# Kernel optimization log

Hardware: AMD Instinct MI355X
Metric: run time of the kernel (lower is better)

## Reference

```python
import jax, jax.numpy as jnp
import numpy as np

BZ, DC, NR = 65536, 512, 1024
MARGIN = 1.0
MASK_VAL = 1000.0

def _l2_normalize(x, eps=1e-12):
    # F.normalize: x / max(||x||_2, eps) along last dim
    n = jnp.sqrt(jnp.sum(x * x, axis=-1, keepdims=True))
    return x / jnp.maximum(n, eps)

def setup_inputs() -> dict:
    key = jax.random.key(0)
    k1, k2, k3 = jax.random.split(key, 3)
    wo = jax.random.normal(k1, (BZ, DC), dtype=jnp.float32)
    rel_weight = jax.random.normal(k2, (NR, DC), dtype=jnp.float32)
    in_y = jax.random.randint(k3, (BZ,), 0, NR, dtype=jnp.int64)
    return {"wo": wo, "rel_weight": rel_weight, "in_y": in_y}

def reference(wo, rel_weight, in_y):
    wo_n = _l2_normalize(wo)                       # [bz, dc]
    rw_n = _l2_normalize(rel_weight)               # [nr, dc]
    # ||a-b|| for unit vectors: sqrt(2 - 2 a.b); avoids [bz,nr,dc] intermediate
    sim = jnp.einsum('bd,nd->bn', wo_n, rw_n)      # [bz, nr]
    all_distance = jnp.sqrt(jnp.maximum(2.0 - 2.0 * sim, 0.0))
    b = jnp.arange(wo.shape[0])
    masked = all_distance.at[b, in_y].add(MASK_VAL)  # mask out the true class
    neg_idx = jnp.argmin(masked, axis=1)           # nearest wrong relation
    # gather instead of one-hot matmul; dist to gathered row equals row of all_distance
    pos_distance = all_distance[b, in_y]
    neg_distance = all_distance[b, neg_idx]
    loss = jnp.mean(pos_distance + jnp.clip(MARGIN - neg_distance, 0.0, 9999.0))
    return loss
```

## Files before the change

kernel.cpp:

```cpp
#include <hip/hip_runtime.h>
#include <hip/hip_bf16.h>
#include <stdint.h>

#define BZc 65536
#define DCc 512
#define NRc 1024

#define BM 128
#define BNC 128
#define BKC 64
#define A_BYTES (BM * DCc * 2)
#define B_BYTES (BNC * BKC * 2)
#define SMEM_BYTES (A_BYTES + B_BYTES + 512 + 512 + 512 + 16)

typedef __bf16 bf16x8 __attribute__((ext_vector_type(8)));
typedef float f32x4 __attribute__((ext_vector_type(4)));

__device__ __forceinline__ unsigned short f2bf(float f) {
    unsigned int u = __float_as_uint(f);
    return (unsigned short)((u + 0x7FFFu + ((u >> 16) & 1u)) >> 16);
}

__global__ void __launch_bounds__(64) ndl_prep_kernel(const float* __restrict__ rw,
                                                      unsigned short* __restrict__ rwn,
                                                      float* __restrict__ out) {
    if (blockIdx.x == 0 && threadIdx.x == 0) out[0] = 0.0f;
    const int t = threadIdx.x;
    const int row = blockIdx.x * 8 + (t >> 3);
    const int l8 = t & 7;
    const float4* src = (const float4*)(rw + (size_t)row * DCc);
    float4 v[16];
    float ss = 0.0f;
#pragma unroll
    for (int i = 0; i < 16; ++i) {
        v[i] = src[l8 + 8 * i];
        ss += v[i].x * v[i].x + v[i].y * v[i].y + v[i].z * v[i].z + v[i].w * v[i].w;
    }
    ss += __shfl_xor(ss, 1);
    ss += __shfl_xor(ss, 2);
    ss += __shfl_xor(ss, 4);
    const float inv = rsqrtf(fmaxf(ss, 1e-24f));
    ushort4* dst = (ushort4*)(rwn + (size_t)row * DCc);
#pragma unroll
    for (int i = 0; i < 16; ++i) {
        ushort4 u;
        u.x = f2bf(v[i].x * inv); u.y = f2bf(v[i].y * inv);
        u.z = f2bf(v[i].z * inv); u.w = f2bf(v[i].w * inv);
        dst[l8 + 8 * i] = u;
    }
}

__global__ void __launch_bounds__(256) ndl_main_kernel(const float* __restrict__ wo,
                                                       const unsigned short* __restrict__ rwn,
                                                       const long long* __restrict__ iy,
                                                       float* __restrict__ out) {
    extern __shared__ char smem[];
    char* Ab = smem;
    char* Bb = smem + A_BYTES;
    unsigned int* rowmax = (unsigned int*)(smem + A_BYTES + B_BYTES);
    float* simY = (float*)(smem + A_BYTES + B_BYTES + 512);
    int* yv = (int*)(smem + A_BYTES + B_BYTES + 1024);
    float* redsum = (float*)(smem + A_BYTES + B_BYTES + 1536);

    const int t = threadIdx.x;
    const int rbase = blockIdx.x * BM;

    if (t < BM) {
        rowmax[t] = 0u;
        simY[t] = 0.0f;
        yv[t] = (int)iy[rbase + t];
    }

    {
        const int l8 = t & 7;
#pragma unroll 1
        for (int p = 0; p < 4; ++p) {
            const int rloc = p * 32 + (t >> 3);
            const float4* src = (const float4*)(wo + (size_t)(rbase + rloc) * DCc);
            float4 v[16];
            float ss = 0.0f;
#pragma unroll
            for (int i = 0; i < 16; ++i) {
                v[i] = src[l8 + 8 * i];
                ss += v[i].x * v[i].x + v[i].y * v[i].y + v[i].z * v[i].z + v[i].w * v[i].w;
            }
            ss += __shfl_xor(ss, 1);
            ss += __shfl_xor(ss, 2);
            ss += __shfl_xor(ss, 4);
            const float inv = rsqrtf(fmaxf(ss, 1e-24f));
            const int swz = (rloc & 7) << 4;
            char* rowp = Ab + rloc * (DCc * 2);
#pragma unroll
            for (int i = 0; i < 16; ++i) {
                ushort4 u;
                u.x = f2bf(v[i].x * inv); u.y = f2bf(v[i].y * inv);
                u.z = f2bf(v[i].z * inv); u.w = f2bf(v[i].w * inv);
                const int boff = ((l8 + 8 * i) * 8) ^ swz;
                *(ushort4*)(rowp + boff) = u;
            }
        }
    }

    const int wid = t >> 6;
    const int lane = t & 63;
    const int wm = wid >> 1;
    const int wn = wid & 1;
    const int lm = lane & 15;
    const int lk = lane >> 4;

    int a_rowbase[4], a_swz[4];
#pragma unroll
    for (int mt = 0; mt < 4; ++mt) {
        const int r = wm * 64 + mt * 16 + lm;
        a_rowbase[mt] = r * (DCc * 2);
        a_swz[mt] = (r & 7) << 4;
    }
    int b_rowbase[4], b_swz[4];
#pragma unroll
    for (int nt = 0; nt < 4; ++nt) {
        const int n = wn * 64 + nt * 16 + lm;
        b_rowbase[nt] = n * (BKC * 2);
        b_swz[nt] = (n & 7) << 4;
    }

    for (int nb = 0; nb < 8; ++nb) {
        f32x4 acc[4][4];
#pragma unroll
        for (int mt = 0; mt < 4; ++mt)
#pragma unroll
            for (int nt = 0; nt < 4; ++nt) {
                f32x4 z = {0.0f, 0.0f, 0.0f, 0.0f};
                acc[mt][nt] = z;
            }

        for (int kb = 0; kb < 8; ++kb) {
            __syncthreads();
            {
                int4 tmp[4];
#pragma unroll
                for (int it = 0; it < 4; ++it) {
                    const int f = it * 256 + t;
                    const int nloc = f >> 3;
                    const int inner = ((f & 7) << 4) ^ ((nloc & 7) << 4);
                    const char* g = (const char*)rwn +
                        (size_t)(nb * BNC + nloc) * (DCc * 2) + kb * (BKC * 2) + inner;
                    tmp[it] = *(const int4*)g;
                }
#pragma unroll
                for (int it = 0; it < 4; ++it) {
                    const int f = it * 256 + t;
                    *(int4*)(Bb + f * 16) = tmp[it];
                }
            }
            __syncthreads();

#pragma unroll
            for (int kk = 0; kk < 2; ++kk) {
                const int koffA = kb * 128 + kk * 64 + lk * 16;
                const int koffB = kk * 64 + lk * 16;
                bf16x8 af[4], bfr[4];
#pragma unroll
                for (int mt = 0; mt < 4; ++mt)
                    af[mt] = *(const bf16x8*)(Ab + a_rowbase[mt] + (koffA ^ a_swz[mt]));
#pragma unroll
                for (int nt = 0; nt < 4; ++nt)
                    bfr[nt] = *(const bf16x8*)(Bb + b_rowbase[nt] + (koffB ^ b_swz[nt]));
#pragma unroll
                for (int mt = 0; mt < 4; ++mt)
#pragma unroll
                    for (int nt = 0; nt < 4; ++nt)
                        acc[mt][nt] = __builtin_amdgcn_mfma_f32_16x16x32_bf16(
                            af[mt], bfr[nt], acc[mt][nt], 0, 0, 0);
            }
        }

#pragma unroll
        for (int mt = 0; mt < 4; ++mt) {
#pragma unroll
            for (int r = 0; r < 4; ++r) {
                const int mloc = wm * 64 + mt * 16 + lk * 4 + r;
                const int y = yv[mloc];
                float mx = -2.0f;
#pragma unroll
                for (int nt = 0; nt < 4; ++nt) {
                    float s = acc[mt][nt][r];
                    const int nglb = nb * BNC + wn * 64 + nt * 16 + lm;
                    if (nglb == y) { simY[mloc] = s; s = -2.0f; }
                    mx = fmaxf(mx, s);
                }
                mx = fmaxf(mx, __shfl_xor(mx, 1));
                mx = fmaxf(mx, __shfl_xor(mx, 2));
                mx = fmaxf(mx, __shfl_xor(mx, 4));
                mx = fmaxf(mx, __shfl_xor(mx, 8));
                if (lm == 0)
                    atomicMax(&rowmax[mloc], __float_as_uint(mx + 2.0f));
            }
        }
    }

    __syncthreads();
    float c = 0.0f;
    if (t < BM) {
        const float ms = __uint_as_float(rowmax[t]) - 2.0f;
        const float sy = simY[t];
        const float pos = sqrtf(fmaxf(2.0f - 2.0f * sy, 0.0f));
        const float neg = sqrtf(fmaxf(2.0f - 2.0f * ms, 0.0f));
        c = pos + fminf(fmaxf(1.0f - neg, 0.0f), 9999.0f);
    }
    c += __shfl_xor(c, 1);
    c += __shfl_xor(c, 2);
    c += __shfl_xor(c, 4);
    c += __shfl_xor(c, 8);
    c += __shfl_xor(c, 16);
    c += __shfl_xor(c, 32);
    if (lane == 0) redsum[wid] = c;
    __syncthreads();
    if (t == 0) {
        const float tot = redsum[0] + redsum[1] + redsum[2] + redsum[3];
        atomicAdd(out, tot * (1.0f / (float)BZc));
    }
}

extern "C" void kernel_launch(void* const* d_in, const int* in_sizes, int n_in,
                              void* d_out, int out_size, void* d_ws, size_t ws_size,
                              hipStream_t stream) {
    const float* wo = (const float*)d_in[0];
    const float* rw = (const float*)d_in[1];
    const long long* iy = (const long long*)d_in[2];
    float* out = (float*)d_out;
    unsigned short* rwn = (unsigned short*)d_ws;

    (void)hipFuncSetAttribute(reinterpret_cast<const void*>(ndl_main_kernel),
                              hipFuncAttributeMaxDynamicSharedMemorySize, SMEM_BYTES);

    ndl_prep_kernel<<<NRc / 8, 64, 0, stream>>>(rw, rwn, out);
    ndl_main_kernel<<<BZc / BM, 256, SMEM_BYTES, stream>>>(wo, rwn, iy, out);
}
```

Before: 359.5 us.

## Switch similarity GEMM to FP8 MFMA with async LDS-pipelined B loads

Replaces the bf16 GEMM with fp8 (e4m3) MFMA on both operands. The wo rows are quantized to fp8 without normalizing first, and the inverse norm is applied afterwards to the row max and the true-class similarity. The block tile shrinks to 64 rows, and B chunks stream straight into LDS through global_load_lds with a 4-deep ring buffer. Per-row max tracking moves into registers, replacing the shared-memory atomics, and launch bounds now target 3 blocks per CU. The goal is to halve operand bytes, double MFMA throughput, and overlap loads with compute. The cost is fp8 precision, which could flip argmin choices among nearby classes and perturb the loss.

```diff
diff --git a/kernel.cpp b/kernel.cpp
--- a/kernel.cpp
+++ b/kernel.cpp
@@ -1,224 +1,220 @@
 #include <hip/hip_runtime.h>
-#include <hip/hip_bf16.h>
 #include <stdint.h>
 
 #define BZc 65536
 #define DCc 512
 #define NRc 1024
-
-#define BM 128
-#define BNC 128
-#define BKC 64
-#define A_BYTES (BM * DCc * 2)
-#define B_BYTES (BNC * BKC * 2)
-#define SMEM_BYTES (A_BYTES + B_BYTES + 512 + 512 + 512 + 16)
-
-typedef __bf16 bf16x8 __attribute__((ext_vector_type(8)));
+#define BM 64
+#define NCHUNK 128
+#define BCH 4096
+
 typedef float f32x4 __attribute__((ext_vector_type(4)));
-
-__device__ __forceinline__ unsigned short f2bf(float f) {
-    unsigned int u = __float_as_uint(f);
-    return (unsigned short)((u + 0x7FFFu + ((u >> 16) & 1u)) >> 16);
-}
-
-__global__ void __launch_bounds__(64) ndl_prep_kernel(const float* __restrict__ rw,
-                                                      unsigned short* __restrict__ rwn,
-                                                      float* __restrict__ out) {
+typedef const unsigned int __attribute__((address_space(1)))* gas1_t;
+typedef unsigned int __attribute__((address_space(3)))* las3_t;
+
+__global__ void __launch_bounds__(64) ndl_prep(const float* __restrict__ rw,
+                                               unsigned char* __restrict__ rwn,
+                                               float* __restrict__ out) {
     if (blockIdx.x == 0 && threadIdx.x == 0) out[0] = 0.0f;
     const int t = threadIdx.x;
     const int row = blockIdx.x * 8 + (t >> 3);
     const int l8 = t & 7;
-    const float4* src = (const float4*)(rw + (size_t)row * DCc);
+    const float4* src = (const float4*)(rw + (size_t)row * DCc) + l8 * 16;
     float4 v[16];
     float ss = 0.0f;
 #pragma unroll
     for (int i = 0; i < 16; ++i) {
-        v[i] = src[l8 + 8 * i];
-        ss += v[i].x * v[i].x + v[i].y * v[i].y + v[i].z * v[i].z + v[i].w * v[i].w;
+        v[i] = src[i];
+        ss += v[i].x*v[i].x + v[i].y*v[i].y + v[i].z*v[i].z + v[i].w*v[i].w;
     }
     ss += __shfl_xor(ss, 1);
     ss += __shfl_xor(ss, 2);
     ss += __shfl_xor(ss, 4);
     const float inv = rsqrtf(fmaxf(ss, 1e-24f));
-    ushort4* dst = (ushort4*)(rwn + (size_t)row * DCc);
-#pragma unroll
-    for (int i = 0; i < 16; ++i) {
-        ushort4 u;
-        u.x = f2bf(v[i].x * inv); u.y = f2bf(v[i].y * inv);
-        u.z = f2bf(v[i].z * inv); u.w = f2bf(v[i].w * inv);
-        dst[l8 + 8 * i] = u;
+    const int swz = ((row >> 2) & 3) << 3;
+    char* rowp = (char*)rwn + (size_t)row * DCc;
+#pragma unroll
+    for (int g = 0; g < 8; ++g) {
+        int lo = __builtin_amdgcn_cvt_pk_fp8_f32(v[2*g].x*inv,   v[2*g].y*inv,   0,  false);
+        lo     = __builtin_amdgcn_cvt_pk_fp8_f32(v[2*g].z*inv,   v[2*g].w*inv,   lo, true);
+        int hi = __builtin_amdgcn_cvt_pk_fp8_f32(v[2*g+1].x*inv, v[2*g+1].y*inv, 0,  false);
+        hi     = __builtin_amdgcn_cvt_pk_fp8_f32(v[2*g+1].z*inv, v[2*g+1].w*inv, hi, true);
+        int2 pk; pk.x = lo; pk.y = hi;
+        *(int2*)(rowp + ((l8 * 64 + g * 8) ^ swz)) = pk;
     }
 }
 
-__global__ void __launch_bounds__(256) ndl_main_kernel(const float* __restrict__ wo,
-                                                       const unsigned short* __restrict__ rwn,
-                                                       const long long* __restrict__ iy,
-                                                       float* __restrict__ out) {
-    extern __shared__ char smem[];
-    char* Ab = smem;
-    char* Bb = smem + A_BYTES;
-    unsigned int* rowmax = (unsigned int*)(smem + A_BYTES + B_BYTES);
-    float* simY = (float*)(smem + A_BYTES + B_BYTES + 512);
-    int* yv = (int*)(smem + A_BYTES + B_BYTES + 1024);
-    float* redsum = (float*)(smem + A_BYTES + B_BYTES + 1536);
+__global__ void __launch_bounds__(256, 3) ndl_main(const float* __restrict__ wo,
+                                                   const unsigned char* __restrict__ rwn,
+                                                   const long long* __restrict__ iy,
+                                                   float* __restrict__ out) {
+    __shared__ char As[BM * DCc];
+    __shared__ char Bs[4 * BCH];
+    __shared__ float invn[BM];
+    __shared__ float mxs[BM];
+    __shared__ float sys[BM];
+    __shared__ float redsum[4];
 
     const int t = threadIdx.x;
-    const int rbase = blockIdx.x * BM;
-
-    if (t < BM) {
-        rowmax[t] = 0u;
-        simY[t] = 0.0f;
-        yv[t] = (int)iy[rbase + t];
-    }
-
-    {
-        const int l8 = t & 7;
-#pragma unroll 1
-        for (int p = 0; p < 4; ++p) {
-            const int rloc = p * 32 + (t >> 3);
-            const float4* src = (const float4*)(wo + (size_t)(rbase + rloc) * DCc);
-            float4 v[16];
-            float ss = 0.0f;
-#pragma unroll
-            for (int i = 0; i < 16; ++i) {
-                v[i] = src[l8 + 8 * i];
-                ss += v[i].x * v[i].x + v[i].y * v[i].y + v[i].z * v[i].z + v[i].w * v[i].w;
-            }
-            ss += __shfl_xor(ss, 1);
-            ss += __shfl_xor(ss, 2);
-            ss += __shfl_xor(ss, 4);
-            const float inv = rsqrtf(fmaxf(ss, 1e-24f));
-            const int swz = (rloc & 7) << 4;
-            char* rowp = Ab + rloc * (DCc * 2);
-#pragma unroll
-            for (int i = 0; i < 16; ++i) {
-                ushort4 u;
-                u.x = f2bf(v[i].x * inv); u.y = f2bf(v[i].y * inv);
-                u.z = f2bf(v[i].z * inv); u.w = f2bf(v[i].w * inv);
-                const int boff = ((l8 + 8 * i) * 8) ^ swz;
-                *(ushort4*)(rowp + boff) = u;
-            }
-        }
-    }
-
     const int wid = t >> 6;
     const int lane = t & 63;
+    const int lm = lane & 15;
+    const int lk = lane >> 4;
     const int wm = wid >> 1;
     const int wn = wid & 1;
-    const int lm = lane & 15;
-    const int lk = lane >> 4;
-
-    int a_rowbase[4], a_swz[4];
-#pragma unroll
-    for (int mt = 0; mt < 4; ++mt) {
-        const int r = wm * 64 + mt * 16 + lm;
-        a_rowbase[mt] = r * (DCc * 2);
-        a_swz[mt] = (r & 7) << 4;
-    }
-    int b_rowbase[4], b_swz[4];
+    const int rbase = blockIdx.x * BM;
+
+    int yrow[2][4];
+#pragma unroll
+    for (int mt = 0; mt < 2; ++mt)
+#pragma unroll
+        for (int r = 0; r < 4; ++r)
+            yrow[mt][r] = (int)iy[rbase + wm*32 + mt*16 + lk*4 + r];
+
+    {
+        const int r = t >> 2;
+        const int q = t & 3;
+        const float* src = wo + (size_t)(rbase + r) * DCc + q * 128;
+        const int swz = (r & 15) << 3;
+        char* rowp = As + r * DCc;
+        float ss = 0.0f;
+#pragma unroll
+        for (int g = 0; g < 16; ++g) {
+            float4 v0 = *(const float4*)(src + g * 8);
+            float4 v1 = *(const float4*)(src + g * 8 + 4);
+            ss += v0.x*v0.x + v0.y*v0.y + v0.z*v0.z + v0.w*v0.w
+                + v1.x*v1.x + v1.y*v1.y + v1.z*v1.z + v1.w*v1.w;
+            int lo = __builtin_amdgcn_cvt_pk_fp8_f32(v0.x, v0.y, 0,  false);
+            lo     = __builtin_amdgcn_cvt_pk_fp8_f32(v0.z, v0.w, lo, true);
+            int hi = __builtin_amdgcn_cvt_pk_fp8_f32(v1.x, v1.y, 0,  false);
+            hi     = __builtin_amdgcn_cvt_pk_fp8_f32(v1.z, v1.w, hi, true);
+            int2 pk; pk.x = lo; pk.y = hi;
+            *(int2*)(rowp + ((q * 128 + g * 8) ^ swz)) = pk;
+        }
+        ss += __shfl_xor(ss, 1);
+        ss += __shfl_xor(ss, 2);
+        if (q == 0) invn[r] = rsqrtf(fmaxf(ss, 1e-24f));
+    }
+    __syncthreads();
+
+    const int r0 = wm*32 + lm;
+    const int r1 = wm*32 + 16 + lm;
+    const int arow0 = r0 * DCc, aswz0 = (r0 & 15) << 3;
+    const int arow1 = r1 * DCc, aswz1 = (r1 & 15) << 3;
+    int boff[4];
 #pragma unroll
     for (int nt = 0; nt < 4; ++nt) {
-        const int n = wn * 64 + nt * 16 + lm;
-        b_rowbase[nt] = n * (BKC * 2);
-        b_swz[nt] = (n & 7) << 4;
-    }
-
-    for (int nb = 0; nb < 8; ++nb) {
-        f32x4 acc[4][4];
-#pragma unroll
-        for (int mt = 0; mt < 4; ++mt)
-#pragma unroll
-            for (int nt = 0; nt < 4; ++nt) {
-                f32x4 z = {0.0f, 0.0f, 0.0f, 0.0f};
-                acc[mt][nt] = z;
+        const int n = wn*64 + nt*16 + lm;
+        boff[nt] = n * 32 + ((lk * 8) ^ (((n >> 2) & 3) << 3));
+    }
+    const unsigned char* bsrc = rwn + (size_t)((wid*32 + (lane >> 1)) * DCc + (lane & 1) * 16);
+    char* bdst = Bs + wid * 1024;
+
+#define ISSUE_B(C) do {                                                          \
+        const int c_ = (C) & (NCHUNK - 1);                                       \
+        __builtin_amdgcn_global_load_lds(                                        \
+            (gas1_t)(bsrc + ((c_ >> 4) << 16) + ((c_ & 15) << 5)),               \
+            (las3_t)(bdst + (c_ & 3) * BCH), 16, 0, 0);                          \
+    } while (0)
+
+    ISSUE_B(0); ISSUE_B(1); ISSUE_B(2);
+
+    f32x4 acc[2][4];
+    float mx[2][4], sy[2][4];
+#pragma unroll
+    for (int mt = 0; mt < 2; ++mt)
+#pragma unroll
+        for (int nt = 0; nt < 4; ++nt) { f32x4 z = {0.f,0.f,0.f,0.f}; acc[mt][nt] = z; }
+#pragma unroll
+    for (int mt = 0; mt < 2; ++mt)
+#pragma unroll
+        for (int r = 0; r < 4; ++r) { mx[mt][r] = -1e30f; sy[mt][r] = -1e30f; }
+
+    for (int c = 0; c < NCHUNK; ++c) {
+        asm volatile("s_waitcnt vmcnt(2) lgkmcnt(0)" ::: "memory");
+        __builtin_amdgcn_s_barrier();
+        __builtin_amdgcn_sched_barrier(0);
+        ISSUE_B(c + 3);
+
+        const int kt = c & 15;
+        const char* bb = Bs + (c & 3) * BCH;
+        const int ka = kt * 32 + lk * 8;
+        unsigned long long a0 = *(const unsigned long long*)(As + arow0 + (ka ^ aswz0));
+        unsigned long long a1 = *(const unsigned long long*)(As + arow1 + (ka ^ aswz1));
+        unsigned long long b0 = *(const unsigned long long*)(bb + boff[0]);
+        unsigned long long b1 = *(const unsigned long long*)(bb + boff[1]);
+        unsigned long long b2 = *(const unsigned long long*)(bb + boff[2]);
+        unsigned long long b3 = *(const unsigned long long*)(bb + boff[3]);
+        acc[0][0] = __builtin_amdgcn_mfma_f32_16x16x32_fp8_fp8(a0, b0, acc[0][0], 0, 0, 0);
+        acc[0][1] = __builtin_amdgcn_mfma_f32_16x16x32_fp8_fp8(a0, b1, acc[0][1], 0, 0, 0);
+        acc[0][2] = __builtin_amdgcn_mfma_f32_16x16x32_fp8_fp8(a0, b2, acc[0][2], 0, 0, 0);
+        acc[0][3] = __builtin_amdgcn_mfma_f32_16x16x32_fp8_fp8(a0, b3, acc[0][3], 0, 0, 0);
+        acc[1][0] = __builtin_amdgcn_mfma_f32_16x16x32_fp8_fp8(a1, b0, acc[1][0], 0, 0, 0);
+        acc[1][1] = __builtin_amdgcn_mfma_f32_16x16x32_fp8_fp8(a1, b1, acc[1][1], 0, 0, 0);
+        acc[1][2] = __builtin_amdgcn_mfma_f32_16x16x32_fp8_fp8(a1, b2, acc[1][2], 0, 0, 0);
+        acc[1][3] = __builtin_amdgcn_mfma_f32_16x16x32_fp8_fp8(a1, b3, acc[1][3], 0, 0, 0);
+
+        if (kt == 15) {
+            const int nb = c >> 4;
+#pragma unroll
+            for (int mt = 0; mt < 2; ++mt)
+#pragma unroll
+                for (int nt = 0; nt < 4; ++nt) {
+                    const int nglb = nb*128 + wn*64 + nt*16 + lm;
+#pragma unroll
+                    for (int r = 0; r < 4; ++r) {
+                        float s = acc[mt][nt][r];
+                        if (nglb == yrow[mt][r]) { sy[mt][r] = s; s = -1e30f; }
+                        mx[mt][r] = fmaxf(mx[mt][r], s);
+                    }
+                    f32x4 z = {0.f,0.f,0.f,0.f};
+                    acc[mt][nt] = z;
+                }
+        }
+    }
+    asm volatile("s_waitcnt vmcnt(0)" ::: "memory");
+
+#pragma unroll
+    for (int d = 1; d <= 8; d <<= 1)
+#pragma unroll
+        for (int mt = 0; mt < 2; ++mt)
+#pragma unroll
+            for (int r = 0; r < 4; ++r) {
+                mx[mt][r] = fmaxf(mx[mt][r], __shfl_xor(mx[mt][r], d));
+                sy[mt][r] = fmaxf(sy[mt][r], __shfl_xor(sy[mt][r], d));
             }
-
-        for (int kb = 0; kb < 8; ++kb) {
-            __syncthreads();
-            {
-                int4 tmp[4];
-#pragma unroll
-                for (int it = 0; it < 4; ++it) {
-                    const int f = it * 256 + t;
-                    const int nloc = f >> 3;
-                    const int inner = ((f & 7) << 4) ^ ((nloc & 7) << 4);
-                    const char* g = (const char*)rwn +
-                        (size_t)(nb * BNC + nloc) * (DCc * 2) + kb * (BKC * 2) + inner;
-                    tmp[it] = *(const int4*)g;
-                }
-#pragma unroll
-                for (int it = 0; it < 4; ++it) {
-                    const int f = it * 256 + t;
-                    *(int4*)(Bb + f * 16) = tmp[it];
-                }
+    if (wn == 0 && lm == 0) {
+#pragma unroll
+        for (int mt = 0; mt < 2; ++mt)
+#pragma unroll
+            for (int r = 0; r < 4; ++r) {
+                const int row = wm*32 + mt*16 + lk*4 + r;
+                mxs[row] = mx[mt][r];
+                sys[row] = sy[mt][r];
             }
-            __syncthreads();
-
-#pragma unroll
-            for (int kk = 0; kk < 2; ++kk) {
-                const int koffA = kb * 128 + kk * 64 + lk * 16;
-                const int koffB = kk * 64 + lk * 16;
-                bf16x8 af[4], bfr[4];
-#pragma unroll
-                for (int mt = 0; mt < 4; ++mt)
-                    af[mt] = *(const bf16x8*)(Ab + a_rowbase[mt] + (koffA ^ a_swz[mt]));
-#pragma unroll
-                for (int nt = 0; nt < 4; ++nt)
-                    bfr[nt] = *(const bf16x8*)(Bb + b_rowbase[nt] + (koffB ^ b_swz[nt]));
-#pragma unroll
-                for (int mt = 0; mt < 4; ++mt)
-#pragma unroll
-                    for (int nt = 0; nt < 4; ++nt)
-                        acc[mt][nt] = __builtin_amdgcn_mfma_f32_16x16x32_bf16(
-                            af[mt], bfr[nt], acc[mt][nt], 0, 0, 0);
+    }
+    __syncthreads();
+    float csum = 0.0f;
+    if (wn == 1 && lm == 0) {
+#pragma unroll
+        for (int mt = 0; mt < 2; ++mt)
+#pragma unroll
+            for (int r = 0; r < 4; ++r) {
+                const int row = wm*32 + mt*16 + lk*4 + r;
+                const float inva = invn[row];
+                const float ms  = fmaxf(mx[mt][r], mxs[row]) * inva;
+                const float syv = fmaxf(sy[mt][r], sys[row]) * inva;
+                const float pos = sqrtf(fmaxf(2.0f - 2.0f * syv, 0.0f));
+                const float neg = sqrtf(fmaxf(2.0f - 2.0f * ms, 0.0f));
+                csum += pos + fminf(fmaxf(1.0f - neg, 0.0f), 9999.0f);
             }
-        }
-
-#pragma unroll
-        for (int mt = 0; mt < 4; ++mt) {
-#pragma unroll
-            for (int r = 0; r < 4; ++r) {
-                const int mloc = wm * 64 + mt * 16 + lk * 4 + r;
-                const int y = yv[mloc];
-                float mx = -2.0f;
-#pragma unroll
-                for (int nt = 0; nt < 4; ++nt) {
-                    float s = acc[mt][nt][r];
-                    const int nglb = nb * BNC + wn * 64 + nt * 16 + lm;
-                    if (nglb == y) { simY[mloc] = s; s = -2.0f; }
-                    mx = fmaxf(mx, s);
-                }
-                mx = fmaxf(mx, __shfl_xor(mx, 1));
-                mx = fmaxf(mx, __shfl_xor(mx, 2));
-                mx = fmaxf(mx, __shfl_xor(mx, 4));
-                mx = fmaxf(mx, __shfl_xor(mx, 8));
-                if (lm == 0)
-                    atomicMax(&rowmax[mloc], __float_as_uint(mx + 2.0f));
-            }
-        }
-    }
-
+    }
+#pragma unroll
+    for (int d = 1; d <= 32; d <<= 1) csum += __shfl_xor(csum, d);
+    if (lane == 0) redsum[wid] = csum;
     __syncthreads();
-    float c = 0.0f;
-    if (t < BM) {
-        const float ms = __uint_as_float(rowmax[t]) - 2.0f;
-        const float sy = simY[t];
-        const float pos = sqrtf(fmaxf(2.0f - 2.0f * sy, 0.0f));
-        const float neg = sqrtf(fmaxf(2.0f - 2.0f * ms, 0.0f));
-        c = pos + fminf(fmaxf(1.0f - neg, 0.0f), 9999.0f);
-    }
-    c += __shfl_xor(c, 1);
-    c += __shfl_xor(c, 2);
-    c += __shfl_xor(c, 4);
-    c += __shfl_xor(c, 8);
-    c += __shfl_xor(c, 16);
-    c += __shfl_xor(c, 32);
-    if (lane == 0) redsum[wid] = c;
-    __syncthreads();
-    if (t == 0) {
-        const float tot = redsum[0] + redsum[1] + redsum[2] + redsum[3];
-        atomicAdd(out, tot * (1.0f / (float)BZc));
-    }
+    if (t == 0)
+        atomicAdd(out, (redsum[0] + redsum[1] + redsum[2] + redsum[3]) * (1.0f / (float)BZc));
 }
 
 extern "C" void kernel_launch(void* const* d_in, const int* in_sizes, int n_in,
@@ -228,11 +224,8 @@
     const float* rw = (const float*)d_in[1];
     const long long* iy = (const long long*)d_in[2];
     float* out = (float*)d_out;
-    unsigned short* rwn = (unsigned short*)d_ws;
-
-    (void)hipFuncSetAttribute(reinterpret_cast<const void*>(ndl_main_kernel),
-                              hipFuncAttributeMaxDynamicSharedMemorySize, SMEM_BYTES);
-
-    ndl_prep_kernel<<<NRc / 8, 64, 0, stream>>>(rw, rwn, out);
-    ndl_main_kernel<<<BZc / BM, 256, SMEM_BYTES, stream>>>(wo, rwn, iy, out);
+    unsigned char* rwn = (unsigned char*)d_ws;
+
+    ndl_prep<<<NRc / 8, 64, 0, stream>>>(rw, rwn, out);
+    ndl_main<<<BZc / BM, 256, 0, stream>>>(wo, rwn, iy, out);
 }
```

Result: faster. 290.1 us (-19.3%).
